# Kernel optimization log

Measured on AMD Instinct MI355X. Metric: run time of the kernel, lower is better.

Reference implementation:

```python
import jax, jax.numpy as jnp
import numpy as np

THETA = 10000.0
EMBED_DIM = 384
NUM_HEADS = 6

def apply_rope_2d(x):
    # x: [B, C, H, W]
    B, C, H, W = x.shape
    dim = C // 2
    inv = 1.0 / THETA ** (jnp.arange(0, dim, 2, dtype=x.dtype) / dim)  # [dim/2]
    fh = jnp.arange(H, dtype=x.dtype)[:, None] * inv[None, :]          # [H, dim/2]
    fw = jnp.arange(W, dtype=x.dtype)[:, None] * inv[None, :]          # [W, dim/2]
    fh_flat = jnp.broadcast_to(fh[:, None, :], (H, W, dim // 2)).reshape(H * W, dim // 2)
    fw_flat = jnp.broadcast_to(fw[None, :, :], (H, W, dim // 2)).reshape(H * W, dim // 2)
    x_seq = x.reshape(B, C, H * W).transpose(0, 2, 1)  # [B, HW, C]
    x_h, x_w = x_seq[..., :dim], x_seq[..., dim:]

    def apply_rotary(t, f):
        # torch stack([c,c],-1).flatten(-2) == repeat each elem twice consecutively
        cos = jnp.repeat(jnp.cos(f), 2, axis=-1)  # [HW, dim]
        sin = jnp.repeat(jnp.sin(f), 2, axis=-1)
        t1, t2 = jnp.split(t, 2, axis=-1)
        rot = jnp.concatenate([-t2, t1], axis=-1)
        return t * cos + rot * sin

    x_h = apply_rotary(x_h, fh_flat)
    x_w = apply_rotary(x_w, fw_flat)
    x_out = jnp.concatenate([x_h, x_w], axis=-1)       # [B, HW, C]
    return x_out.transpose(0, 2, 1).reshape(B, C, H, W)

def conv1x1(x, W, b):
    # 1x1 conv == channel matmul
    return jnp.einsum('oc,bchw->bohw', W, x) + b[None, :, None, None]

def setup_inputs() -> dict:
    key = jax.random.key(0)
    ks = jax.random.split(key, 9)
    B, C, H, W = 8, EMBED_DIM, 64, 64
    s = 1.0 / np.sqrt(C)
    inp = {'x': jax.random.normal(ks[0], (B, C, H, W), dtype=jnp.float32)}
    for i, name in enumerate(['q', 'k', 'v', 'fc']):
        inp[f'W{name}'] = jax.random.uniform(ks[1 + 2 * i], (C, C), dtype=jnp.float32, minval=-s, maxval=s)
        inp[f'b{name}'] = jax.random.uniform(ks[2 + 2 * i], (C,), dtype=jnp.float32, minval=-s, maxval=s)
    return inp

def reference(x, Wq, bq, Wk, bk, Wv, bv, Wfc, bfc):
    B, C, H, W = x.shape
    nh = NUM_HEADS
    hd = C // nh
    scale = hd ** -0.5
    q = apply_rope_2d(conv1x1(x, Wq, bq))
    k = apply_rope_2d(conv1x1(x, Wk, bk))
    v = conv1x1(x, Wv, bv)
    # [B, nh, HW, hd]
    def to_heads(t):
        return t.reshape(B, nh, hd, H * W).transpose(0, 1, 3, 2)
    q = jax.nn.elu(to_heads(q) * scale) + 1.0
    k = jax.nn.elu(to_heads(k)) + 1.0
    v = to_heads(v)
    kv = jnp.einsum('bhnd,bhne->bhde', k, v)               # [B, nh, hd, hd]
    k_sum = k.sum(axis=2)                                   # [B, nh, hd]
    normalizer = jnp.einsum('bhnd,bhd->bhn', q, k_sum)[..., None]
    out = jnp.einsum('bhnd,bhde->bhne', q, kv) / (normalizer + 1e-6)
    out = out.transpose(0, 1, 3, 2).reshape(B, C, H, W)
    return conv1x1(out, Wfc, bfc)
```

## Files before the change

kernel.cpp:

```cpp
#include <hip/hip_runtime.h>
#include <math.h>

#define BATCH 8
#define CCH 384
#define NPIX 4096
#define NHEADS 6
#define SZ ((size_t)BATCH * CCH * NPIX)

typedef __attribute__((ext_vector_type(8))) short short8;
typedef __attribute__((ext_vector_type(4))) float f32x4;

__device__ __forceinline__ float elu1(float x) { return x > 0.f ? x + 1.f : expf(x); }

__device__ __forceinline__ unsigned short bf16_rne(float f) {
    unsigned u = __builtin_bit_cast(unsigned, f);
    u += 0x7FFFu + ((u >> 16) & 1u);
    return (unsigned short)(u >> 16);
}
__device__ __forceinline__ float bf16_f(unsigned short h) {
    return __builtin_bit_cast(float, ((unsigned)h) << 16);
}
__device__ __forceinline__ unsigned packsplit(float v) {
    unsigned short hi = bf16_rne(v);
    unsigned short lo = bf16_rne(v - bf16_f(hi));
    return ((unsigned)hi << 16) | (unsigned)lo;
}

__global__ __launch_bounds__(256) void pack_x_kernel(
    const float* __restrict__ X, unsigned* __restrict__ Xp)
{
    size_t i = ((size_t)blockIdx.x * 256 + threadIdx.x) * 4;
    float4 v = *(const float4*)(X + i);
    uint4 o;
    o.x = packsplit(v.x); o.y = packsplit(v.y);
    o.z = packsplit(v.z); o.w = packsplit(v.w);
    *(uint4*)(Xp + i) = o;
}

__global__ __launch_bounds__(256) void trig_kernel(float2* __restrict__ T)
{
    const float KC = 0.13841367062030680f;
    int idx = blockIdx.x * 256 + threadIdx.x;
    int f = idx >> 6, pos = idx & 63;
    float ang = (float)pos * exp2f(-KC * (float)f);
    float s, c;
    sincosf(ang, &s, &c);
    T[idx] = make_float2(s, c);
}

__global__ __launch_bounds__(256) void pack_w_kernel(
    const float* __restrict__ Wq, const float* __restrict__ Wk,
    const float* __restrict__ Wv, const float* __restrict__ Wfc,
    unsigned short* __restrict__ Wp)
{
    const int tid = threadIdx.x;
    const int lane = tid & 63;
    const int f = blockIdx.x * 4 + (tid >> 6);
    const int rloc = lane & 15;
    const int ks = (lane >> 4) * 8;

    const float* Wsel;
    int ch;
    if (f < 72) {
        int which = f / 24;
        int r = (f % 24) * 16 + rloc;
        if (which < 2) {
            int u = r >> 1;
            int cu = (u < 96) ? u : u + 96;
            ch = cu + 96 * (r & 1);
        } else {
            ch = r;
        }
        Wsel = (which == 0) ? Wq : (which == 1) ? Wk : Wv;
    } else {
        ch = (f - 72) * 16 + rloc;
        Wsel = Wfc;
    }

    for (int c = 0; c < 12; ++c) {
        short8 hv, lv;
#pragma unroll
        for (int j = 0; j < 8; ++j) {
            float v = Wsel[(size_t)ch * CCH + c * 32 + ks + j];
            unsigned short h = bf16_rne(v);
            hv[j] = (short)h;
            lv[j] = (short)bf16_rne(v - bf16_f(h));
        }
        size_t off = (size_t)f * 12288 + (size_t)c * 1024 + (size_t)lane * 8;
        *(short8*)(Wp + off) = hv;
        *(short8*)(Wp + off + 512) = lv;
    }
}

template <int MODE>
__global__ __launch_bounds__(256, 2) void mfma_gemm(
    const unsigned* __restrict__ Xin,
    const unsigned short* __restrict__ Wp,
    const float2* __restrict__ Ttab,
    const float* __restrict__ b0, const float* __restrict__ b1, const float* __restrict__ b2,
    float* __restrict__ O0, float* __restrict__ O1, float* __restrict__ O2)
{
    __shared__ unsigned Bs[32][129];

    const int tid = threadIdx.x;
    const int lane = tid & 63;
    const int wave = tid >> 6;
    const int wm = wave >> 1, wn = wave & 1;
    const int mt = blockIdx.y * 2 + wm;
    const int nblk = blockIdx.x;
    const int b = blockIdx.z;
    const int g = lane >> 4;
    const int ln = lane & 15;

    f32x4 acc[4][4] = {};

    const int sr = tid >> 3;
    const int sc = (tid & 7) * 16;
    const unsigned* sbase = Xin + (size_t)b * CCH * NPIX + nblk * 128 + sc;
    const unsigned short* wbase = Wp + (size_t)(mt * 4) * 12288 + (size_t)lane * 8;

#pragma unroll 1
    for (int c = 0; c < 12; ++c) {
        __syncthreads();
        {
            const unsigned* src = sbase + (size_t)(c * 32 + sr) * NPIX;
            uint4 v0 = *(const uint4*)(src + 0);
            uint4 v1 = *(const uint4*)(src + 4);
            uint4 v2 = *(const uint4*)(src + 8);
            uint4 v3 = *(const uint4*)(src + 12);
            Bs[sr][sc + 0]  = v0.x; Bs[sr][sc + 1]  = v0.y;
            Bs[sr][sc + 2]  = v0.z; Bs[sr][sc + 3]  = v0.w;
            Bs[sr][sc + 4]  = v1.x; Bs[sr][sc + 5]  = v1.y;
            Bs[sr][sc + 6]  = v1.z; Bs[sr][sc + 7]  = v1.w;
            Bs[sr][sc + 8]  = v2.x; Bs[sr][sc + 9]  = v2.y;
            Bs[sr][sc + 10] = v2.z; Bs[sr][sc + 11] = v2.w;
            Bs[sr][sc + 12] = v3.x; Bs[sr][sc + 13] = v3.y;
            Bs[sr][sc + 14] = v3.z; Bs[sr][sc + 15] = v3.w;
        }
        __syncthreads();

        short8 ah[4], al[4];
#pragma unroll
        for (int i = 0; i < 4; ++i) {
            const unsigned short* p = wbase + (size_t)i * 12288 + c * 1024;
            ah[i] = *(const short8*)(p);
            al[i] = *(const short8*)(p + 512);
        }

#pragma unroll
        for (int jj = 0; jj < 4; ++jj) {
            const int col = wn * 64 + jj * 16 + ln;
            short8 bh, bl;
#pragma unroll
            for (int j = 0; j < 8; ++j) {
                unsigned uu = Bs[g * 8 + j][col];
                bh[j] = (short)(uu >> 16);
                bl[j] = (short)(uu & 0xFFFFu);
            }
#pragma unroll
            for (int i = 0; i < 4; ++i) {
                acc[i][jj] = __builtin_amdgcn_mfma_f32_16x16x32_bf16(ah[i], bh, acc[i][jj], 0, 0, 0);
                acc[i][jj] = __builtin_amdgcn_mfma_f32_16x16x32_bf16(ah[i], bl, acc[i][jj], 0, 0, 0);
                acc[i][jj] = __builtin_amdgcn_mfma_f32_16x16x32_bf16(al[i], bh, acc[i][jj], 0, 0, 0);
            }
        }
    }

    const int ncol0 = nblk * 128 + wn * 64 + ln;

    if (MODE == 1) {
#pragma unroll
        for (int i = 0; i < 4; ++i) {
            const int rowb = mt * 64 + i * 16 + g * 4;
#pragma unroll
            for (int r = 0; r < 4; ++r) {
                const int row = rowb + r;
                const float bias = b0[row];
                float* orow = O0 + ((size_t)b * CCH + row) * NPIX;
#pragma unroll
                for (int jj = 0; jj < 4; ++jj)
                    orow[ncol0 + jj * 16] = acc[i][jj][r] + bias;
            }
        }
    } else {
        const int which = mt / 6;
        const int mloc = (mt % 6) * 64;
        const float* bsel = (which == 0) ? b0 : (which == 1) ? b1 : b2;
        float* osel = (which == 0) ? O0 : (which == 1) ? O1 : O2;
        if (which == 2) {
#pragma unroll
            for (int i = 0; i < 4; ++i) {
                const int rowb = mloc + i * 16 + g * 4;
#pragma unroll
                for (int r = 0; r < 4; ++r) {
                    const int row = rowb + r;
                    const float bias = bsel[row];
                    float* orow = osel + ((size_t)b * CCH + row) * NPIX;
#pragma unroll
                    for (int jj = 0; jj < 4; ++jj)
                        orow[ncol0 + jj * 16] = acc[i][jj][r] + bias;
                }
            }
        } else {
            const float qs = (which == 0) ? 0.125f : 1.0f;
            const int posH = nblk * 2 + wn;
#pragma unroll
            for (int i = 0; i < 4; ++i) {
#pragma unroll
                for (int p = 0; p < 2; ++p) {
                    const int re = mloc + i * 16 + g * 4 + 2 * p;
                    const int u = re >> 1;
                    const bool isH = (u < 96);
                    const int cu = isH ? u : u + 96;
                    const int jA = isH ? (u >> 1) : ((u - 96) >> 1);
                    const float be = bsel[cu];
                    const float bo = bsel[cu + 96];
                    float* orE = osel + ((size_t)b * CCH + cu) * NPIX;
                    float* orO = orE + (size_t)96 * NPIX;
                    const float2* Ta = Ttab + jA * 64;
                    const float2* Tb = Ttab + (jA + 48) * 64;
                    if (isH) {
                        const float2 fa = Ta[posH];
                        const float2 fb = Tb[posH];
#pragma unroll
                        for (int jj = 0; jj < 4; ++jj) {
                            const int n = ncol0 + jj * 16;
                            const float te = acc[i][jj][2 * p] + be;
                            const float to = acc[i][jj][2 * p + 1] + bo;
                            orE[n] = elu1((te * fa.y - to * fa.x) * qs);
                            orO[n] = elu1((to * fb.y + te * fb.x) * qs);
                        }
                    } else {
#pragma unroll
                        for (int jj = 0; jj < 4; ++jj) {
                            const int n = ncol0 + jj * 16;
                            const int pw = jj * 16 + ln;
                            const float2 fa = Ta[pw];
                            const float2 fb = Tb[pw];
                            const float te = acc[i][jj][2 * p] + be;
                            const float to = acc[i][jj][2 * p + 1] + bo;
                            orE[n] = elu1((te * fa.y - to * fa.x) * qs);
                            orO[n] = elu1((to * fb.y + te * fb.x) * qs);
                        }
                    }
                }
            }
        }
    }
}

__global__ __launch_bounds__(256) void kv_kernel(
    const float* __restrict__ Kin, const float* __restrict__ Vin,
    float* __restrict__ KV, float* __restrict__ KS)
{
    __shared__ float Ks[32][68];
    __shared__ float Vs[32][68];
    const int tid = threadIdx.x;
    const int bh = blockIdx.x;
    const int ns = blockIdx.y;
    const int b = bh / NHEADS, h = bh % NHEADS;
    const float* kb = Kin + ((size_t)b * CCH + h * 64) * NPIX;
    const float* vb = Vin + ((size_t)b * CCH + h * 64) * NPIX;
    const int drow = tid >> 2;
    const int nl = (tid & 3) * 8;
    const int td = (tid & 15) * 4;
    const int te = (tid >> 4) * 4;

    float acc[4][4];
    float ks[4] = {0.f, 0.f, 0.f, 0.f};
#pragma unroll
    for (int i = 0; i < 4; ++i)
#pragma unroll
        for (int j = 0; j < 4; ++j) acc[i][j] = 0.f;

    for (int n0 = ns * 256; n0 < ns * 256 + 256; n0 += 32) {
        __syncthreads();
        const float* kr = kb + (size_t)drow * NPIX + n0 + nl;
        const float* vr = vb + (size_t)drow * NPIX + n0 + nl;
        float4 k0 = *(const float4*)kr;
        float4 k1 = *(const float4*)(kr + 4);
        float4 v0 = *(const float4*)vr;
        float4 v1 = *(const float4*)(vr + 4);
        Ks[nl + 0][drow] = k0.x; Ks[nl + 1][drow] = k0.y;
        Ks[nl + 2][drow] = k0.z; Ks[nl + 3][drow] = k0.w;
        Ks[nl + 4][drow] = k1.x; Ks[nl + 5][drow] = k1.y;
        Ks[nl + 6][drow] = k1.z; Ks[nl + 7][drow] = k1.w;
        Vs[nl + 0][drow] = v0.x; Vs[nl + 1][drow] = v0.y;
        Vs[nl + 2][drow] = v0.z; Vs[nl + 3][drow] = v0.w;
        Vs[nl + 4][drow] = v1.x; Vs[nl + 5][drow] = v1.y;
        Vs[nl + 6][drow] = v1.z; Vs[nl + 7][drow] = v1.w;
        __syncthreads();
#pragma unroll 8
        for (int nn = 0; nn < 32; ++nn) {
            float4 a = *(const float4*)&Ks[nn][td];
            float4 w = *(const float4*)&Vs[nn][te];
            float av[4] = {a.x, a.y, a.z, a.w};
            float wv[4] = {w.x, w.y, w.z, w.w};
            ks[0] += av[0]; ks[1] += av[1]; ks[2] += av[2]; ks[3] += av[3];
#pragma unroll
            for (int i = 0; i < 4; ++i)
#pragma unroll
                for (int j = 0; j < 4; ++j) acc[i][j] += av[i] * wv[j];
        }
    }

    float* kvb = KV + (size_t)bh * 64 * 64;
#pragma unroll
    for (int i = 0; i < 4; ++i)
#pragma unroll
        for (int j = 0; j < 4; ++j)
            atomicAdd(&kvb[(td + i) * 64 + (te + j)], acc[i][j]);
    if (te == 0) {
#pragma unroll
        for (int i = 0; i < 4; ++i) atomicAdd(&KS[bh * 64 + td + i], ks[i]);
    }
}

__global__ __launch_bounds__(256) void attn_kernel(
    const float* __restrict__ Q, const float* __restrict__ KV,
    const float* __restrict__ KS, unsigned* __restrict__ O)
{
    __shared__ float Qs[64][132];
    __shared__ float KVs[64][64];
    __shared__ float KSs[64];
    const int tid = threadIdx.x;
    const int n0 = blockIdx.x * 128;
    const int bh = blockIdx.y;
    const int b = bh / NHEADS, h = bh % NHEADS;
    const float* qb = Q + ((size_t)b * CCH + h * 64) * NPIX;

    {
        const int row = tid >> 2;
        const int c0 = (tid & 3) * 32;
        const float* qr = qb + (size_t)row * NPIX + n0 + c0;
#pragma unroll
        for (int j = 0; j < 8; ++j)
            *(float4*)&Qs[row][c0 + j * 4] = *(const float4*)&qr[j * 4];
        const int kc = (tid & 3) * 16;
        const float* kvr = KV + (size_t)bh * 4096 + (size_t)row * 64 + kc;
#pragma unroll
        for (int j = 0; j < 4; ++j)
            *(float4*)&KVs[row][kc + j * 4] = *(const float4*)&kvr[j * 4];
        if (tid < 64) KSs[tid] = KS[bh * 64 + tid];
    }
    __syncthreads();

    const int tx = tid & 31;
    const int ty = tid >> 5;
    float acc[8][4];
    float accn[4] = {0.f, 0.f, 0.f, 0.f};
#pragma unroll
    for (int r = 0; r < 8; ++r)
#pragma unroll
        for (int j = 0; j < 4; ++j) acc[r][j] = 0.f;

#pragma unroll 8
    for (int d = 0; d < 64; ++d) {
        float4 qv = *(const float4*)&Qs[d][tx * 4];
        float qa[4] = {qv.x, qv.y, qv.z, qv.w};
        float ksv = KSs[d];
#pragma unroll
        for (int j = 0; j < 4; ++j) accn[j] += ksv * qa[j];
        float4 k0 = *(const float4*)&KVs[d][ty * 8];
        float4 k1 = *(const float4*)&KVs[d][ty * 8 + 4];
        float kva[8] = {k0.x, k0.y, k0.z, k0.w, k1.x, k1.y, k1.z, k1.w};
#pragma unroll
        for (int r = 0; r < 8; ++r)
#pragma unroll
            for (int j = 0; j < 4; ++j) acc[r][j] += kva[r] * qa[j];
    }

    float rcp[4];
#pragma unroll
    for (int j = 0; j < 4; ++j) rcp[j] = 1.f / (accn[j] + 1e-6f);
#pragma unroll
    for (int r = 0; r < 8; ++r) {
        unsigned* orow = O + ((size_t)b * CCH + h * 64 + ty * 8 + r) * NPIX + n0 + tx * 4;
        uint4 o4;
        o4.x = packsplit(acc[r][0] * rcp[0]);
        o4.y = packsplit(acc[r][1] * rcp[1]);
        o4.z = packsplit(acc[r][2] * rcp[2]);
        o4.w = packsplit(acc[r][3] * rcp[3]);
        *(uint4*)orow = o4;
    }
}

__global__ void zero_kernel(float* p, int n)
{
    int i = blockIdx.x * blockDim.x + threadIdx.x;
    if (i < n) p[i] = 0.f;
}

extern "C" void kernel_launch(void* const* d_in, const int* in_sizes, int n_in,
                              void* d_out, int out_size, void* d_ws, size_t ws_size,
                              hipStream_t stream)
{
    const float* x   = (const float*)d_in[0];
    const float* Wq  = (const float*)d_in[1];
    const float* bq  = (const float*)d_in[2];
    const float* Wk  = (const float*)d_in[3];
    const float* bk  = (const float*)d_in[4];
    const float* Wv  = (const float*)d_in[5];
    const float* bv  = (const float*)d_in[6];
    const float* Wfc = (const float*)d_in[7];
    const float* bfc = (const float*)d_in[8];
    float* out = (float*)d_out;
    float* ws = (float*)d_ws;

    float* q    = ws;
    float* k    = ws + SZ;
    float* v    = ws + 2 * SZ;
    float* kv   = ws + 3 * SZ;
    float* ksum = kv + 48 * 64 * 64;
    float2* Ttab = (float2*)(ksum + 48 * 64);
    unsigned short* Wp = (unsigned short*)(Ttab + 96 * 64);
    unsigned* xp = (unsigned*)d_out;
    unsigned* op = (unsigned*)k;

    const int nz = 48 * 64 * 64 + 48 * 64;
    zero_kernel<<<(nz + 255) / 256, 256, 0, stream>>>(kv, nz);
    trig_kernel<<<24, 256, 0, stream>>>(Ttab);
    pack_w_kernel<<<24, 256, 0, stream>>>(Wq, Wk, Wv, Wfc, Wp);
    pack_x_kernel<<<(int)(SZ / 1024), 256, 0, stream>>>(x, xp);
    mfma_gemm<0><<<dim3(32, 9, BATCH), 256, 0, stream>>>(xp, Wp, Ttab, bq, bk, bv, q, k, v);
    kv_kernel<<<dim3(48, 16), 256, 0, stream>>>(k, v, kv, ksum);
    attn_kernel<<<dim3(32, 48), 256, 0, stream>>>(q, kv, ksum, op);
    mfma_gemm<1><<<dim3(32, 3, BATCH), 256, 0, stream>>>(op, Wp + (size_t)72 * 12288, Ttab,
                                                         bfc, bfc, bfc, out, out, out);
}
```

Baseline: 354.7 us.

## Fuse x bf16 split-packing into QKV GEMM and swizzle LDS tile

Removes the separate pack_x kernel and converts fp32 x to hi/lo bf16 pairs while staging tiles into shared memory in the QKV GEMM. The LDS tile drops row padding in favour of an XOR swizzle, which enables 128-bit LDS stores and avoids bank conflicts on the column reads. This saves a full read and write pass over x. In exchange, each block redoes the split conversion for every M-tile.

```diff
diff --git a/kernel.cpp b/kernel.cpp
--- a/kernel.cpp
+++ b/kernel.cpp
@@ -26,15 +26,8 @@
     return ((unsigned)hi << 16) | (unsigned)lo;
 }
 
-__global__ __launch_bounds__(256) void pack_x_kernel(
-    const float* __restrict__ X, unsigned* __restrict__ Xp)
-{
-    size_t i = ((size_t)blockIdx.x * 256 + threadIdx.x) * 4;
-    float4 v = *(const float4*)(X + i);
-    uint4 o;
-    o.x = packsplit(v.x); o.y = packsplit(v.y);
-    o.z = packsplit(v.z); o.w = packsplit(v.w);
-    *(uint4*)(Xp + i) = o;
+__device__ __forceinline__ int bswz(int idx, int k) {
+    return idx ^ ((k & 7) << 2) ^ (((k >> 3) & 1) << 4);
 }
 
 __global__ __launch_bounds__(256) void trig_kernel(float2* __restrict__ T)
@@ -94,13 +87,13 @@
 
 template <int MODE>
 __global__ __launch_bounds__(256, 2) void mfma_gemm(
-    const unsigned* __restrict__ Xin,
+    const void* __restrict__ Xin,
     const unsigned short* __restrict__ Wp,
     const float2* __restrict__ Ttab,
     const float* __restrict__ b0, const float* __restrict__ b1, const float* __restrict__ b2,
     float* __restrict__ O0, float* __restrict__ O1, float* __restrict__ O2)
 {
-    __shared__ unsigned Bs[32][129];
+    __shared__ unsigned Bs[32 * 128];
 
     const int tid = threadIdx.x;
     const int lane = tid & 63;
@@ -116,26 +109,43 @@
 
     const int sr = tid >> 3;
     const int sc = (tid & 7) * 16;
-    const unsigned* sbase = Xin + (size_t)b * CCH * NPIX + nblk * 128 + sc;
+    const int swx = ((sr & 7) << 2) | (((sr >> 3) & 1) << 4);
     const unsigned short* wbase = Wp + (size_t)(mt * 4) * 12288 + (size_t)lane * 8;
+
+    const float* sbF = (const float*)Xin + (size_t)b * CCH * NPIX + nblk * 128 + sc;
+    const unsigned* sbU = (const unsigned*)Xin + (size_t)b * CCH * NPIX + nblk * 128 + sc;
 
 #pragma unroll 1
     for (int c = 0; c < 12; ++c) {
         __syncthreads();
-        {
-            const unsigned* src = sbase + (size_t)(c * 32 + sr) * NPIX;
+        if (MODE == 0) {
+            const float* src = sbF + (size_t)(c * 32 + sr) * NPIX;
+            float vals[16];
+            *(float4*)&vals[0]  = *(const float4*)(src + 0);
+            *(float4*)&vals[4]  = *(const float4*)(src + 4);
+            *(float4*)&vals[8]  = *(const float4*)(src + 8);
+            *(float4*)&vals[12] = *(const float4*)(src + 12);
+            const int rb = sr * 128 + sc;
+#pragma unroll
+            for (int w = 0; w < 4; ++w) {
+                uint4 o;
+                o.x = packsplit(vals[w * 4 + 0]);
+                o.y = packsplit(vals[w * 4 + 1]);
+                o.z = packsplit(vals[w * 4 + 2]);
+                o.w = packsplit(vals[w * 4 + 3]);
+                *(uint4*)&Bs[(rb + 4 * w) ^ swx] = o;
+            }
+        } else {
+            const unsigned* src = sbU + (size_t)(c * 32 + sr) * NPIX;
             uint4 v0 = *(const uint4*)(src + 0);
             uint4 v1 = *(const uint4*)(src + 4);
             uint4 v2 = *(const uint4*)(src + 8);
             uint4 v3 = *(const uint4*)(src + 12);
-            Bs[sr][sc + 0]  = v0.x; Bs[sr][sc + 1]  = v0.y;
-            Bs[sr][sc + 2]  = v0.z; Bs[sr][sc + 3]  = v0.w;
-            Bs[sr][sc + 4]  = v1.x; Bs[sr][sc + 5]  = v1.y;
-            Bs[sr][sc + 6]  = v1.z; Bs[sr][sc + 7]  = v1.w;
-            Bs[sr][sc + 8]  = v2.x; Bs[sr][sc + 9]  = v2.y;
-            Bs[sr][sc + 10] = v2.z; Bs[sr][sc + 11] = v2.w;
-            Bs[sr][sc + 12] = v3.x; Bs[sr][sc + 13] = v3.y;
-            Bs[sr][sc + 14] = v3.z; Bs[sr][sc + 15] = v3.w;
+            const int rb = sr * 128 + sc;
+            *(uint4*)&Bs[(rb + 0)  ^ swx] = v0;
+            *(uint4*)&Bs[(rb + 4)  ^ swx] = v1;
+            *(uint4*)&Bs[(rb + 8)  ^ swx] = v2;
+            *(uint4*)&Bs[(rb + 12) ^ swx] = v3;
         }
         __syncthreads();
 
@@ -153,7 +163,8 @@
             short8 bh, bl;
 #pragma unroll
             for (int j = 0; j < 8; ++j) {
-                unsigned uu = Bs[g * 8 + j][col];
+                const int k = g * 8 + j;
+                unsigned uu = Bs[(k * 128 + col) ^ ((j & 7) << 2) ^ (((g & 1)) << 4)];
                 bh[j] = (short)(uu >> 16);
                 bl[j] = (short)(uu & 0xFFFFu);
             }
@@ -414,15 +425,13 @@
     float* ksum = kv + 48 * 64 * 64;
     float2* Ttab = (float2*)(ksum + 48 * 64);
     unsigned short* Wp = (unsigned short*)(Ttab + 96 * 64);
-    unsigned* xp = (unsigned*)d_out;
     unsigned* op = (unsigned*)k;
 
     const int nz = 48 * 64 * 64 + 48 * 64;
     zero_kernel<<<(nz + 255) / 256, 256, 0, stream>>>(kv, nz);
     trig_kernel<<<24, 256, 0, stream>>>(Ttab);
     pack_w_kernel<<<24, 256, 0, stream>>>(Wq, Wk, Wv, Wfc, Wp);
-    pack_x_kernel<<<(int)(SZ / 1024), 256, 0, stream>>>(x, xp);
-    mfma_gemm<0><<<dim3(32, 9, BATCH), 256, 0, stream>>>(xp, Wp, Ttab, bq, bk, bv, q, k, v);
+    mfma_gemm<0><<<dim3(32, 9, BATCH), 256, 0, stream>>>(x, Wp, Ttab, bq, bk, bv, q, k, v);
     kv_kernel<<<dim3(48, 16), 256, 0, stream>>>(k, v, kv, ksum);
     attn_kernel<<<dim3(32, 48), 256, 0, stream>>>(q, kv, ksum, op);
     mfma_gemm<1><<<dim3(32, 3, BATCH), 256, 0, stream>>>(op, Wp + (size_t)72 * 12288, Ttab,
```

Result: slower. 362.0 us (+2.1%).
